# Performance work log

Measured on AMD Instinct MI355X. Metric: run time of the kernel, lower is better.

Reference implementation:

```python
import math
import jax, jax.numpy as jnp
import numpy as np

N = 50000      # nodes
E = 600000     # edges (before self-loops)
D_IN = 64
COND = 32
B = 50         # cond batch; N % B == 0
DT = 128       # dim_t
DH = 128       # dim_h
L = 3          # num GAT layers
FD = 16        # learned_sinusoidal_dim


def setup_inputs() -> dict:
    key = jax.random.key(0)
    ks = jax.random.split(key, 32)
    p = lambda k, shp: (jax.random.normal(k, shp, jnp.float32) * 0.05)
    return {
        "x": jax.random.normal(ks[0], (N, D_IN), jnp.float32),
        "adj": jax.random.randint(ks[1], (2, E), 0, N, dtype=jnp.int32),
        "ef": jax.random.normal(ks[2], (E, 8), jnp.float32),
        "timesteps": jax.random.uniform(ks[3], (N,), jnp.float32) * 1000.0,
        "cond": jax.random.normal(ks[4], (B, COND), jnp.float32),
        # random fourier weights (fixed, not trained in original since is_random=True)
        "fourier_w": jax.random.normal(ks[5], (FD // 2,), jnp.float32),
        # time MLP: Linear(FD+1, DT) -> SiLU -> Linear(DT, DT)
        "tW1": p(ks[6], (FD + 1, DT)), "tb1": p(ks[7], (DT,)),
        "tW2": p(ks[8], (DT, DT)),   "tb2": p(ks[9], (DT,)),
        # conditional projections
        "pxW": p(ks[10], (D_IN, DT)), "pxb": p(ks[11], (DT,)),
        "pcW": p(ks[12], (COND, DT)), "pcb": p(ks[13], (DT,)),
        # stacked GATConv params (all layers 128->128, heads=1)
        "linW": p(ks[14], (L, DT, DH)),   # lin, bias=False
        "attS": p(ks[15], (L, DH)),       # att_src
        "attD": p(ks[16], (L, DH)),       # att_dst
        "gbias": p(ks[17], (L, DH)),      # GATConv bias
        "resW": p(ks[18], (L, DT, DH)),   # residual Linear, bias=False
        # decode MLP
        "dW1": p(ks[19], (DH, DH)), "db1": p(ks[20], (DH,)),
        "dW2": p(ks[21], (DH, 2)),  "db2": p(ks[22], (2,)),
    }


def _gat_layer(h, src, dst, n, linW, attS, attD, gbias, resW):
    # PyG GATConv, heads=1, concat=True, residual=True, add_self_loops already in src/dst
    xl = h @ linW                          # [n, DH]
    a_src = xl @ attS                      # [n]
    a_dst = xl @ attD                      # [n]
    e = jax.nn.leaky_relu(a_src[src] + a_dst[dst], 0.2)   # [E2]
    m = jax.ops.segment_max(e, dst, num_segments=n)
    w = jnp.exp(e - m[dst])
    den = jax.ops.segment_sum(w, dst, num_segments=n)
    alpha = w / den[dst]                   # softmax per destination node
    out = jax.ops.segment_sum(alpha[:, None] * xl[src], dst, num_segments=n)
    return out + gbias + h @ resW


def reference(x, adj, ef, timesteps, cond, fourier_w, tW1, tb1, tW2, tb2,
              pxW, pxb, pcW, pcb, linW, attS, attD, gbias, resW,
              dW1, db1, dW2, db2):
    n = x.shape[0]
    # time embedding: random fourier features, dim = FD + 1
    t = timesteps[:, None]
    freqs = t * fourier_w[None, :] * (2.0 * math.pi)
    four = jnp.concatenate([t, jnp.sin(freqs), jnp.cos(freqs)], axis=-1)
    temb = jax.nn.silu(four @ tW1 + tb1) @ tW2 + tb2
    # conditional projection (cond repeated to match nodes)
    c = jnp.repeat(cond, n // cond.shape[0], axis=0)
    h = (x @ pxW + pxb) + (c @ pcW + pcb) + temb
    # add self-loops once (PyG GATConv default add_self_loops=True)
    loop = jnp.arange(n, dtype=adj.dtype)
    src = jnp.concatenate([adj[0], loop])
    dst = jnp.concatenate([adj[1], loop])
    for l in range(linW.shape[0]):
        h = _gat_layer(h, src, dst, n, linW[l], attS[l], attD[l], gbias[l], resW[l])
        h = jax.nn.gelu(h, approximate=False)
    # decode MLP
    h = jax.nn.gelu(h @ dW1 + db1, approximate=False)
    return h @ dW2 + db2
```

## Files before the change

### kernel.cpp

```cpp
#include <hip/hip_runtime.h>
#include <hip/hip_bf16.h>

#define N_NODES 50000
#define N_EDGES 600000
#define TOT_EDGES (N_EDGES + N_NODES)
#define NPB 1000
#define SCAN_BLK 49

#define PREP_T0 1563
#define PREP_T1 (PREP_T0 + 544)
#define PREP_T2 (PREP_T1 + 3125)
#define PREP_T3 (PREP_T2 + 25)
#define PREP_T4 (PREP_T3 + 3)

typedef __bf16 bf16x8 __attribute__((ext_vector_type(8)));
typedef float f32x4 __attribute__((ext_vector_type(4)));
typedef unsigned short u16x8 __attribute__((ext_vector_type(8)));

__device__ __forceinline__ float gelu_exact(float v){
  return 0.5f * v * (1.f + erff(v * 0.70710678118654752f));
}
__device__ __forceinline__ float silu(float v){
  return v / (1.f + expf(-v));
}
__device__ __forceinline__ unsigned short f2bf(float f){
  unsigned u = __builtin_bit_cast(unsigned, f);
  unsigned r = (u + 0x7FFFu + ((u >> 16) & 1u)) >> 16;
  return (unsigned short)r;
}
__device__ __forceinline__ float bf2f(unsigned short u){
  return __builtin_bit_cast(float, ((unsigned)u) << 16);
}

__global__ __launch_bounds__(256) void count_deg(const int* __restrict__ adj,
                                                 int* __restrict__ counts,
                                                 int* __restrict__ rank){
  int t = blockIdx.x*256 + threadIdx.x;
  if (t >= N_EDGES/4) return;
  int j4 = t*4;
  const int4 d4 = *(const int4*)&adj[N_EDGES + j4];
  int4 r4;
  r4.x = atomicAdd(&counts[d4.x], 1);
  r4.y = atomicAdd(&counts[d4.y], 1);
  r4.z = atomicAdd(&counts[d4.z], 1);
  r4.w = atomicAdd(&counts[d4.w], 1);
  *(int4*)&rank[j4] = r4;
}

__global__ __launch_bounds__(256) void scan_part(const int* __restrict__ counts, int* __restrict__ blksum){
  int tid = threadIdx.x;
  int base = blockIdx.x*1024 + tid*4;
  int s = 0;
  #pragma unroll
  for (int k = 0; k < 4; k++){ int idx = base+k; if (idx < N_NODES) s += counts[idx] + 1; }
  #pragma unroll
  for (int off = 1; off < 64; off <<= 1) s += __shfl_xor(s, off, 64);
  __shared__ int ws[4];
  int lane = tid & 63, wid = tid >> 6;
  if (lane == 0) ws[wid] = s;
  __syncthreads();
  if (tid == 0) blksum[blockIdx.x] = ws[0]+ws[1]+ws[2]+ws[3];
}

__global__ __launch_bounds__(256) void scan_final(const int* __restrict__ counts,
                                                  const int* __restrict__ blksum,
                                                  int* __restrict__ offsets,
                                                  int* __restrict__ srt_src){
  int tid = threadIdx.x; int lane = tid & 63, wid = tid >> 6;
  __shared__ int ws[4];
  __shared__ int sbase;
  int base = blockIdx.x*1024 + tid*4;
  int v[4]; int s = 0;
  #pragma unroll
  for (int k = 0; k < 4; k++){ int idx = base+k; v[k] = (idx < N_NODES) ? (counts[idx] + 1) : 0; s += v[k]; }
  int x = s;
  #pragma unroll
  for (int off = 1; off < 64; off <<= 1){
    int y = __shfl_up(x, off, 64);
    if (lane >= off) x += y;
  }
  if (lane == 63) ws[wid] = x;
  if (tid < 64){
    int bv = (tid < SCAN_BLK) ? blksum[tid] : 0;
    int bx = bv;
    #pragma unroll
    for (int off = 1; off < 64; off <<= 1){
      int y = __shfl_up(bx, off, 64);
      if (tid >= off) bx += y;
    }
    int basev = (blockIdx.x == 0) ? 0 : __shfl(bx, blockIdx.x - 1, 64);
    int total = __shfl(bx, SCAN_BLK - 1, 64);
    if (tid == 0){
      sbase = basev;
      if (blockIdx.x == SCAN_BLK-1) offsets[N_NODES] = total;
    }
  }
  __syncthreads();
  int run = sbase;
  for (int q = 0; q < wid; q++) run += ws[q];
  run += x - s;
  #pragma unroll
  for (int k = 0; k < 4; k++){
    int idx = base+k;
    if (idx < N_NODES){
      offsets[idx] = run;
      srt_src[run] = idx;
    }
    run += v[k];
  }
}

__global__ __launch_bounds__(256) void scatter_edges(const int* __restrict__ adj,
                                                     const int* __restrict__ rank,
                                                     const int* __restrict__ offsets,
                                                     int* __restrict__ srt_src){
  int t = blockIdx.x*256 + threadIdx.x;
  if (t >= N_EDGES/4) return;
  int j4 = t*4;
  const int4 s4 = *(const int4*)&adj[j4];
  const int4 d4 = *(const int4*)&adj[N_EDGES + j4];
  const int4 r4 = *(const int4*)&rank[j4];
  srt_src[offsets[d4.x] + 1 + r4.x] = s4.x;
  srt_src[offsets[d4.y] + 1 + r4.y] = s4.y;
  srt_src[offsets[d4.z] + 1 + r4.z] = s4.z;
  srt_src[offsets[d4.w] + 1 + r4.w] = s4.w;
}

__global__ __launch_bounds__(256) void prep_all(const float* __restrict__ timesteps,
                                                const float* __restrict__ fw,
                                                const float* __restrict__ tW1,
                                                const float* __restrict__ tb1,
                                                unsigned short* __restrict__ hid,
                                                const float* __restrict__ linW,
                                                const float* __restrict__ resW,
                                                const float* __restrict__ tW2,
                                                const float* __restrict__ pxW,
                                                const float* __restrict__ dW1,
                                                unsigned short* __restrict__ Bt2,
                                                unsigned short* __restrict__ Bt_init,
                                                unsigned short* __restrict__ Bt_d1,
                                                const float* __restrict__ x,
                                                unsigned short* __restrict__ xbf,
                                                const float* __restrict__ cond,
                                                const float* __restrict__ pcW,
                                                const float* __restrict__ pcb,
                                                float* __restrict__ cproj,
                                                const float* __restrict__ attS,
                                                const float* __restrict__ attD,
                                                float* __restrict__ uv){
  __shared__ float sfour[32][17];
  __shared__ float sW[17][128];
  const int bid = blockIdx.x, tid = threadIdx.x;

  if (bid < PREP_T0){
    int row0 = bid * 32;
    if (tid < 32){
      int gr = row0 + tid;
      float t = (gr < N_NODES) ? timesteps[gr] : 0.f;
      sfour[tid][0] = t;
      #pragma unroll
      for (int q = 0; q < 8; q++){
        float f = t * fw[q] * 6.2831853071795864769f;
        float sv, cv;
        sincosf(f, &sv, &cv);
        sfour[tid][1+q] = sv;
        sfour[tid][9+q] = cv;
      }
    }
    for (int i = tid; i < 17*128; i += 256) sW[i>>7][i&127] = tW1[i];
    __syncthreads();
    int j = tid & 127, rg = tid >> 7;
    float b = tb1[j];
    #pragma unroll
    for (int r = 0; r < 16; r++){
      int row = rg*16 + r;
      float acc = b;
      #pragma unroll
      for (int k = 0; k < 17; k++) acc += sfour[row][k]*sW[k][j];
      int gr = row0 + row;
      if (gr < N_NODES) hid[gr*128 + j] = f2bf(silu(acc));
    }
  } else if (bid < PREP_T1){
    int idx = (bid - PREP_T0)*256 + tid;
    if (idx < 98304){
      int j = idx >> 14, e = idx & 16383;
      int l = j >> 1, isres = j & 1;
      int k = e >> 7, c = e & 127;
      const float* src = (isres ? resW : linW) + l*16384;
      Bt2[(size_t)l*32768 + (size_t)(isres*128 + c)*128 + k] = f2bf(src[k*128 + c]);
    } else if (idx < 114688){
      int e = idx - 98304; int k = e >> 7, c = e & 127;
      Bt_init[c*192 + k] = f2bf(tW2[k*128 + c]);
    } else if (idx < 122880){
      int e = idx - 114688; int k = e >> 7, c = e & 127;
      Bt_init[c*192 + 128 + k] = f2bf(pxW[k*128 + c]);
    } else if (idx < 139264){
      int e = idx - 122880; int k = e >> 7, c = e & 127;
      Bt_d1[c*128 + k] = f2bf(dW1[k*128 + c]);
    }
  } else if (bid < PREP_T2){
    int i = (bid - PREP_T1)*256 + tid;
    float4 v = ((const float4*)x)[i];
    ushort4 o;
    o.x = f2bf(v.x); o.y = f2bf(v.y); o.z = f2bf(v.z); o.w = f2bf(v.w);
    *(ushort4*)&xbf[(size_t)i*4] = o;
  } else if (bid < PREP_T3){
    int g = (bid - PREP_T2)*256 + tid;
    int b = g >> 7, j = g & 127;
    float acc = pcb[j];
    for (int k = 0; k < 32; k++) acc += cond[b*32+k]*pcW[k*128+j];
    cproj[b*128+j] = acc;
  } else {
    int g = (bid - PREP_T3)*256 + tid;
    if (g < 768){
      int l = g >> 8, s = (g >> 7) & 1, k = g & 127;
      const float* att = s ? (attD + l*128) : (attS + l*128);
      const float* row = linW + (l*128 + k)*128;
      float acc = 0.f;
      for (int j = 0; j < 128; j++) acc += row[j]*att[j];
      uv[(l*2 + s)*128 + k] = acc;
    }
  }
}

template<int KD, int NC, int EPI, bool DOTS>
__global__ __launch_bounds__(256) void mfma_gemm(const unsigned short* __restrict__ A0,
                                                 const unsigned short* __restrict__ A1,
                                                 const unsigned short* __restrict__ Bt,
                                                 const float* __restrict__ bias0,
                                                 const float* __restrict__ bias1,
                                                 const float* __restrict__ cproj,
                                                 unsigned short* __restrict__ O0,
                                                 unsigned short* __restrict__ O1,
                                                 const float* __restrict__ uv_l,
                                                 float* __restrict__ a_srcO,
                                                 float* __restrict__ a_dstO){
  constexpr int CHR  = KD / 8;
  constexpr int ROWB = KD * 2;
  constexpr int KS   = KD / 32;
  constexpr int NT   = NC / 16;
  __shared__ alignas(16) char sA[64 * ROWB];
  __shared__ alignas(16) char sB[NC * ROWB];
  const int tid  = threadIdx.x;
  const int m0   = blockIdx.x * 64;
  const int lane = tid & 63, w = tid >> 6;
  const int lr   = lane & 15, lk = lane >> 4;

  for (int i = tid; i < 64*CHR; i += 256){
    int r = i / CHR, ch = i % CHR;
    int grow = m0 + r;
    u16x8 v;
    #pragma unroll
    for (int q = 0; q < 8; q++) v[q] = 0;
    if (grow < N_NODES){
      if constexpr (KD == 128){
        v = *(const u16x8*)&A0[(size_t)grow*128 + ch*8];
      } else {
        if (ch < 16) v = *(const u16x8*)&A0[(size_t)grow*128 + ch*8];
        else         v = *(const u16x8*)&A1[(size_t)grow*64 + (ch-16)*8];
      }
    }
    *(u16x8*)&sA[r*ROWB + ((ch*16) ^ ((r & 7) << 4))] = v;
  }
  for (int i = tid; i < NC*CHR; i += 256){
    int r = i / CHR, ch = i % CHR;
    u16x8 v = *(const u16x8*)&Bt[(size_t)r*KD + ch*8];
    *(u16x8*)&sB[r*ROWB + ((ch*16) ^ ((r & 7) << 4))] = v;
  }
  __syncthreads();

  bf16x8 afr[KS];
  const int arow = w*16 + lr;
  #pragma unroll
  for (int ks = 0; ks < KS; ks++)
    afr[ks] = *(const bf16x8*)&sA[arow*ROWB + ((ks*64 + lk*16) ^ ((arow & 7) << 4))];

  f32x4 acc[NT];
  #pragma unroll
  for (int nt = 0; nt < NT; nt++)
    #pragma unroll
    for (int q = 0; q < 4; q++) acc[nt][q] = 0.f;

  #pragma unroll
  for (int nt = 0; nt < NT; nt++){
    const int brow = nt*16 + lr;
    #pragma unroll
    for (int ks = 0; ks < KS; ks++){
      bf16x8 b = *(const bf16x8*)&sB[brow*ROWB + ((ks*64 + lk*16) ^ ((brow & 7) << 4))];
      acc[nt] = __builtin_amdgcn_mfma_f32_16x16x32_bf16(afr[ks], b, acc[nt], 0, 0, 0);
    }
  }

  if constexpr (DOTS){
    int r = tid >> 2;
    int row = m0 + r;
    if (row < N_NODES){
      float ps = 0.f, pd = 0.f;
      #pragma unroll
      for (int cc = 0; cc < 4; cc++){
        int ch = (tid & 3)*4 + cc;
        u16x8 av = *(const u16x8*)&sA[r*ROWB + ((ch*16) ^ ((r & 7) << 4))];
        int c0 = ch*8;
        const float4 u0 = *(const float4*)&uv_l[c0];
        const float4 u1 = *(const float4*)&uv_l[c0+4];
        const float4 v0 = *(const float4*)&uv_l[128+c0];
        const float4 v1 = *(const float4*)&uv_l[128+c0+4];
        const float uu[8] = {u0.x,u0.y,u0.z,u0.w,u1.x,u1.y,u1.z,u1.w};
        const float vv[8] = {v0.x,v0.y,v0.z,v0.w,v1.x,v1.y,v1.z,v1.w};
        #pragma unroll
        for (int q = 0; q < 8; q++){
          float hv = bf2f(av[q]);
          ps += hv*uu[q];
          pd += hv*vv[q];
        }
      }
      ps += __shfl_xor(ps, 1, 64); ps += __shfl_xor(ps, 2, 64);
      pd += __shfl_xor(pd, 1, 64); pd += __shfl_xor(pd, 2, 64);
      if ((tid & 3) == 0){ a_srcO[row] = ps; a_dstO[row] = pd; }
    }
  }

  const int rbase = m0 + w*16 + lk*4;
  #pragma unroll
  for (int nt = 0; nt < NT; nt++){
    int c = nt*16 + lr;
    #pragma unroll
    for (int rg = 0; rg < 4; rg++){
      int row = rbase + rg;
      if (row >= N_NODES) continue;
      float v = acc[nt][rg];
      if constexpr (EPI == 0){
        if (c < 128) O0[(size_t)row*128 + c]       = f2bf(v);
        else         O1[(size_t)row*128 + (c-128)] = f2bf(v);
      } else if constexpr (EPI == 1){
        v += bias0[c] + bias1[c] + cproj[(row/NPB)*128 + c];
        O0[(size_t)row*128 + c] = f2bf(v);
      } else {
        v = gelu_exact(v + bias0[c]);
        O0[(size_t)row*128 + c] = f2bf(v);
      }
    }
  }
}

template<bool FUSE>
__global__ __launch_bounds__(256) void aggregate(const unsigned short* __restrict__ xl,
                                                 const float* __restrict__ a_src,
                                                 const float* __restrict__ a_dst,
                                                 const unsigned short* __restrict__ hres,
                                                 const float* __restrict__ gbias_l,
                                                 const int* __restrict__ offsets,
                                                 const int* __restrict__ srt_src,
                                                 unsigned short* __restrict__ h_out,
                                                 const float* __restrict__ uv_next,
                                                 float* __restrict__ a_src_o,
                                                 float* __restrict__ a_dst_o){
  const int tid  = threadIdx.x;
  const int lane = tid & 63;
  const int l16  = lane & 15;
  const int i    = blockIdx.x*16 + (tid >> 4);
  const int beg  = offsets[i];
  const int deg  = offsets[i+1] - beg;
  const float adst = a_dst[i];

  int   s0  = 0;
  float ev0 = -INFINITY;
  if (l16 < deg){
    s0 = srt_src[beg + l16];
    float t = a_src[s0] + adst;
    ev0 = (t > 0.f) ? t : 0.2f*t;
  }
  float m = ev0;
  #pragma unroll
  for (int off = 1; off < 16; off <<= 1) m = fmaxf(m, __shfl_xor(m, off, 64));
  float den = (l16 < deg) ? __expf(ev0 - m) : 0.f;
  #pragma unroll
  for (int off = 1; off < 16; off <<= 1) den += __shfl_xor(den, off, 64);
  for (int c0 = 16; c0 < deg; c0 += 16){
    float ev = -INFINITY;
    if (c0 + l16 < deg){
      int s = srt_src[beg + c0 + l16];
      float t = a_src[s] + adst;
      ev = (t > 0.f) ? t : 0.2f*t;
    }
    float cm = ev;
    #pragma unroll
    for (int off = 1; off < 16; off <<= 1) cm = fmaxf(cm, __shfl_xor(cm, off, 64));
    if (cm > m){ den *= __expf(m - cm); m = cm; }
    float wv = (c0 + l16 < deg) ? __expf(ev - m) : 0.f;
    #pragma unroll
    for (int off = 1; off < 16; off <<= 1) wv += __shfl_xor(wv, off, 64);
    den += wv;
  }
  const float inv = 1.f / den;
  float w0 = (l16 < deg) ? __expf(ev0 - m) * inv : 0.f;

  float acc[8];
  #pragma unroll
  for (int k = 0; k < 8; k++) acc[k] = 0.f;
  const int gbb = (lane & 48) << 2;

  int lim0 = deg < 16 ? deg : 16;
  for (int q = 0; q < lim0; q++){
    int addr = gbb + q*4;
    int s    = __builtin_amdgcn_ds_bpermute(addr, s0);
    float wq = __builtin_bit_cast(float, __builtin_amdgcn_ds_bpermute(addr, __builtin_bit_cast(int, w0)));
    const int4 xv = *(const int4*)&xl[((size_t)s << 7) + (l16 << 3)];
    const int xd[4] = {xv.x, xv.y, xv.z, xv.w};
    #pragma unroll
    for (int k = 0; k < 4; k++){
      acc[2*k]   += wq * __builtin_bit_cast(float, xd[k] << 16);
      acc[2*k+1] += wq * __builtin_bit_cast(float, xd[k] & 0xffff0000);
    }
  }
  for (int c0 = 16; c0 < deg; c0 += 16){
    int s1 = 0; float w1 = 0.f;
    if (c0 + l16 < deg){
      s1 = srt_src[beg + c0 + l16];
      float t = a_src[s1] + adst;
      float ev = (t > 0.f) ? t : 0.2f*t;
      w1 = __expf(ev - m) * inv;
    }
    int lim = deg - c0; if (lim > 16) lim = 16;
    for (int q = 0; q < lim; q++){
      int addr = gbb + q*4;
      int s    = __builtin_amdgcn_ds_bpermute(addr, s1);
      float wq = __builtin_bit_cast(float, __builtin_amdgcn_ds_bpermute(addr, __builtin_bit_cast(int, w1)));
      const int4 xv = *(const int4*)&xl[((size_t)s << 7) + (l16 << 3)];
      const int xd[4] = {xv.x, xv.y, xv.z, xv.w};
      #pragma unroll
      for (int k = 0; k < 4; k++){
        acc[2*k]   += wq * __builtin_bit_cast(float, xd[k] << 16);
        acc[2*k+1] += wq * __builtin_bit_cast(float, xd[k] & 0xffff0000);
      }
    }
  }

  const int4 hr = *(const int4*)&hres[((size_t)i << 7) + (l16 << 3)];
  const int hd[4] = {hr.x, hr.y, hr.z, hr.w};
  const float4 gb0 = *(const float4*)&gbias_l[l16*8];
  const float4 gb1 = *(const float4*)&gbias_l[l16*8 + 4];
  const float gbv[8] = {gb0.x, gb0.y, gb0.z, gb0.w, gb1.x, gb1.y, gb1.z, gb1.w};
  float uu[8], vv[8];
  if constexpr (FUSE){
    const float4 a0 = *(const float4*)&uv_next[l16*8];
    const float4 a1 = *(const float4*)&uv_next[l16*8 + 4];
    const float4 b0 = *(const float4*)&uv_next[128 + l16*8];
    const float4 b1 = *(const float4*)&uv_next[128 + l16*8 + 4];
    uu[0]=a0.x; uu[1]=a0.y; uu[2]=a0.z; uu[3]=a0.w; uu[4]=a1.x; uu[5]=a1.y; uu[6]=a1.z; uu[7]=a1.w;
    vv[0]=b0.x; vv[1]=b0.y; vv[2]=b0.z; vv[3]=b0.w; vv[4]=b1.x; vv[5]=b1.y; vv[6]=b1.z; vv[7]=b1.w;
  }
  float ps = 0.f, pd = 0.f;
  int od[4];
  #pragma unroll
  for (int k = 0; k < 4; k++){
    float r0 = acc[2*k]   + gbv[2*k]   + __builtin_bit_cast(float, hd[k] << 16);
    float r1 = acc[2*k+1] + gbv[2*k+1] + __builtin_bit_cast(float, hd[k] & 0xffff0000);
    float g0 = gelu_exact(r0);
    float g1 = gelu_exact(r1);
    if constexpr (FUSE){
      ps += g0*uu[2*k] + g1*uu[2*k+1];
      pd += g0*vv[2*k] + g1*vv[2*k+1];
    }
    unsigned lo = f2bf(g0);
    unsigned hi = f2bf(g1);
    od[k] = (int)(lo | (hi << 16));
  }
  *(int4*)&h_out[((size_t)i << 7) + (l16 << 3)] = make_int4(od[0], od[1], od[2], od[3]);
  if constexpr (FUSE){
    #pragma unroll
    for (int off = 1; off < 16; off <<= 1){
      ps += __shfl_xor(ps, off, 64);
      pd += __shfl_xor(pd, off, 64);
    }
    if (l16 == 0){ a_src_o[i] = ps; a_dst_o[i] = pd; }
  }
}

__global__ __launch_bounds__(256) void head2(const unsigned short* __restrict__ g,
                                             const float* __restrict__ dW2,
                                             const float* __restrict__ db2,
                                             float* __restrict__ out){
  const int tid = threadIdx.x;
  const int l16 = tid & 15;
  const int i   = blockIdx.x*16 + (tid >> 4);
  const int4 gv = *(const int4*)&g[((size_t)i << 7) + (l16 << 3)];
  const int gd[4] = {gv.x, gv.y, gv.z, gv.w};
  float wk[16];
  #pragma unroll
  for (int q = 0; q < 4; q++){
    const float4 wq = *(const float4*)&dW2[l16*16 + q*4];
    wk[q*4+0]=wq.x; wk[q*4+1]=wq.y; wk[q*4+2]=wq.z; wk[q*4+3]=wq.w;
  }
  float p0 = 0.f, p1 = 0.f;
  #pragma unroll
  for (int k = 0; k < 4; k++){
    float lo = __builtin_bit_cast(float, gd[k] << 16);
    float hi = __builtin_bit_cast(float, gd[k] & 0xffff0000);
    p0 += lo*wk[4*k+0] + hi*wk[4*k+2];
    p1 += lo*wk[4*k+1] + hi*wk[4*k+3];
  }
  #pragma unroll
  for (int off = 1; off < 16; off <<= 1){
    p0 += __shfl_xor(p0, off, 64);
    p1 += __shfl_xor(p1, off, 64);
  }
  if (l16 == 0){
    float2 o; o.x = p0 + db2[0]; o.y = p1 + db2[1];
    *(float2*)&out[i*2] = o;
  }
}

extern "C" void kernel_launch(void* const* d_in, const int* in_sizes, int n_in,
                              void* d_out, int out_size, void* d_ws, size_t ws_size,
                              hipStream_t stream) {
  const float* x   = (const float*)d_in[0];
  const int*   adj = (const int*)  d_in[1];
  const float* timesteps = (const float*)d_in[3];
  const float* cond = (const float*)d_in[4];
  const float* fw   = (const float*)d_in[5];
  const float* tW1  = (const float*)d_in[6];
  const float* tb1  = (const float*)d_in[7];
  const float* tW2  = (const float*)d_in[8];
  const float* tb2  = (const float*)d_in[9];
  const float* pxW  = (const float*)d_in[10];
  const float* pxb  = (const float*)d_in[11];
  const float* pcW  = (const float*)d_in[12];
  const float* pcb  = (const float*)d_in[13];
  const float* linW = (const float*)d_in[14];
  const float* attS = (const float*)d_in[15];
  const float* attD = (const float*)d_in[16];
  const float* gbias= (const float*)d_in[17];
  const float* resW = (const float*)d_in[18];
  const float* dW1  = (const float*)d_in[19];
  const float* db1  = (const float*)d_in[20];
  const float* dW2  = (const float*)d_in[21];
  const float* db2  = (const float*)d_in[22];
  float* out = (float*)d_out;

  char* w = (char*)d_ws;
  size_t off = 0;
  auto carve = [&](size_t bytes) -> void* {
    void* p = w + off;
    off = (off + bytes + 255) & ~(size_t)255;
    return p;
  };
  unsigned short* h_bf    = (unsigned short*)carve((size_t)N_NODES*128*2);
  unsigned short* xl_bf   = (unsigned short*)carve((size_t)N_NODES*128*2);
  unsigned short* hres_bf = (unsigned short*)carve((size_t)N_NODES*128*2);
  unsigned short* x_bf    = (unsigned short*)carve((size_t)N_NODES*64*2);
  float* a_src0 = (float*)carve((size_t)N_NODES*4);
  float* a_dst0 = (float*)carve((size_t)N_NODES*4);
  float* a_src1 = (float*)carve((size_t)N_NODES*4);
  float* a_dst1 = (float*)carve((size_t)N_NODES*4);
  float* cproj = (float*)carve(50*128*4);
  float* uv    = (float*)carve(6*128*4);
  int* counts  = (int*)carve((size_t)N_NODES*4);
  int* rank    = (int*)carve((size_t)N_EDGES*4);
  int* offsets = (int*)carve((size_t)(N_NODES+1)*4);
  int* srt_src = (int*)carve((size_t)TOT_EDGES*4);
  int* blksum  = (int*)carve(SCAN_BLK*4);
  unsigned short* Bt2     = (unsigned short*)carve((size_t)3*256*128*2);
  unsigned short* Bt_init = (unsigned short*)carve((size_t)128*192*2);
  unsigned short* Bt_d1   = (unsigned short*)carve((size_t)128*128*2);
  (void)ws_size; (void)in_sizes; (void)n_in; (void)out_size;

  const int edge4_blocks = (N_EDGES/4 + 255)/256;
  const int gemm_gx      = (N_NODES + 63)/64;
  const int grp_blocks   = N_NODES/16;

  hipMemsetAsync(counts, 0, (size_t)N_NODES*4, stream);
  count_deg<<<edge4_blocks, 256, 0, stream>>>(adj, counts, rank);
  scan_part<<<SCAN_BLK, 256, 0, stream>>>(counts, blksum);
  scan_final<<<SCAN_BLK, 256, 0, stream>>>(counts, blksum, offsets, srt_src);
  scatter_edges<<<edge4_blocks, 256, 0, stream>>>(adj, rank, offsets, srt_src);

  prep_all<<<PREP_T4, 256, 0, stream>>>(timesteps, fw, tW1, tb1, xl_bf ,
                                        linW, resW, tW2, pxW, dW1, Bt2, Bt_init, Bt_d1,
                                        x, x_bf, cond, pcW, pcb, cproj, attS, attD, uv);

  mfma_gemm<192,128,1,false><<<gemm_gx, 256, 0, stream>>>(xl_bf , x_bf, Bt_init, tb2, pxb, cproj, h_bf, nullptr, nullptr, nullptr, nullptr);

  float* asrc_in = a_src0; float* adst_in = a_dst0;
  float* asrc_out = a_src1; float* adst_out = a_dst1;
  for (int l = 0; l < 3; l++){
    if (l == 0){
      mfma_gemm<128,256,0,true><<<gemm_gx, 256, 0, stream>>>(h_bf, nullptr, Bt2, nullptr, nullptr, nullptr, xl_bf, hres_bf, uv, asrc_in, adst_in);
    } else {
      mfma_gemm<128,256,0,false><<<gemm_gx, 256, 0, stream>>>(h_bf, nullptr, Bt2 + (size_t)l*32768, nullptr, nullptr, nullptr, xl_bf, hres_bf, nullptr, nullptr, nullptr);
    }
    if (l < 2){
      aggregate<true><<<grp_blocks, 256, 0, stream>>>(xl_bf, asrc_in, adst_in, hres_bf, gbias + l*128,
                                                      offsets, srt_src, h_bf, uv + (l+1)*256, asrc_out, adst_out);
      float* t0 = asrc_in; asrc_in = asrc_out; asrc_out = t0;
      float* t1 = adst_in; adst_in = adst_out; adst_out = t1;
    } else {
      aggregate<false><<<grp_blocks, 256, 0, stream>>>(xl_bf, asrc_in, adst_in, hres_bf, gbias + l*128,
                                                       offsets, srt_src, h_bf, nullptr, nullptr, nullptr);
    }
  }

  mfma_gemm<128,128,2,false><<<gemm_gx, 256, 0, stream>>>(h_bf, nullptr, Bt_d1, db1, nullptr, nullptr, xl_bf , nullptr, nullptr, nullptr, nullptr);
  head2<<<grp_blocks, 256, 0, stream>>>(xl_bf , dW2, db2, out);
}
```

Measured before the change: 409.7 us.

## Merge edge counting into prep, scatter into init GEMM, head into decode GEMM

Degree counting now runs as extra blocks of the prep kernel, and the edge scatter runs as extra blocks of the initial projection GEMM launch. The final decode GEMM gains an epilogue that applies GELU and the 128->2 projection in registers, which removes the separate head kernel and the bf16 round-trip of the decoded hidden state. The aim is fewer launches and less global traffic. The cost is more heterogeneous blocks per launch and larger kernel parameter lists.

```diff
diff --git a/kernel.cpp b/kernel.cpp
--- a/kernel.cpp
+++ b/kernel.cpp
@@ -6,12 +6,14 @@
 #define TOT_EDGES (N_EDGES + N_NODES)
 #define NPB 1000
 #define SCAN_BLK 49
-
-#define PREP_T0 1563
-#define PREP_T1 (PREP_T0 + 544)
-#define PREP_T2 (PREP_T1 + 3125)
-#define PREP_T3 (PREP_T2 + 25)
-#define PREP_T4 (PREP_T3 + 3)
+#define GEMM_GX 782
+#define CD_BLKS 586
+
+#define PC_T0 (CD_BLKS + 1563)
+#define PC_T1 (PC_T0 + 544)
+#define PC_T2 (PC_T1 + 3125)
+#define PC_T3 (PC_T2 + 25)
+#define PC_T4 (PC_T3 + 3)
 
 typedef __bf16 bf16x8 __attribute__((ext_vector_type(8)));
 typedef float f32x4 __attribute__((ext_vector_type(4)));
@@ -32,128 +34,49 @@
   return __builtin_bit_cast(float, ((unsigned)u) << 16);
 }
 
-__global__ __launch_bounds__(256) void count_deg(const int* __restrict__ adj,
-                                                 int* __restrict__ counts,
-                                                 int* __restrict__ rank){
-  int t = blockIdx.x*256 + threadIdx.x;
-  if (t >= N_EDGES/4) return;
-  int j4 = t*4;
-  const int4 d4 = *(const int4*)&adj[N_EDGES + j4];
-  int4 r4;
-  r4.x = atomicAdd(&counts[d4.x], 1);
-  r4.y = atomicAdd(&counts[d4.y], 1);
-  r4.z = atomicAdd(&counts[d4.z], 1);
-  r4.w = atomicAdd(&counts[d4.w], 1);
-  *(int4*)&rank[j4] = r4;
-}
-
-__global__ __launch_bounds__(256) void scan_part(const int* __restrict__ counts, int* __restrict__ blksum){
-  int tid = threadIdx.x;
-  int base = blockIdx.x*1024 + tid*4;
-  int s = 0;
-  #pragma unroll
-  for (int k = 0; k < 4; k++){ int idx = base+k; if (idx < N_NODES) s += counts[idx] + 1; }
-  #pragma unroll
-  for (int off = 1; off < 64; off <<= 1) s += __shfl_xor(s, off, 64);
-  __shared__ int ws[4];
-  int lane = tid & 63, wid = tid >> 6;
-  if (lane == 0) ws[wid] = s;
-  __syncthreads();
-  if (tid == 0) blksum[blockIdx.x] = ws[0]+ws[1]+ws[2]+ws[3];
-}
-
-__global__ __launch_bounds__(256) void scan_final(const int* __restrict__ counts,
-                                                  const int* __restrict__ blksum,
-                                                  int* __restrict__ offsets,
-                                                  int* __restrict__ srt_src){
-  int tid = threadIdx.x; int lane = tid & 63, wid = tid >> 6;
-  __shared__ int ws[4];
-  __shared__ int sbase;
-  int base = blockIdx.x*1024 + tid*4;
-  int v[4]; int s = 0;
-  #pragma unroll
-  for (int k = 0; k < 4; k++){ int idx = base+k; v[k] = (idx < N_NODES) ? (counts[idx] + 1) : 0; s += v[k]; }
-  int x = s;
-  #pragma unroll
-  for (int off = 1; off < 64; off <<= 1){
-    int y = __shfl_up(x, off, 64);
-    if (lane >= off) x += y;
-  }
-  if (lane == 63) ws[wid] = x;
-  if (tid < 64){
-    int bv = (tid < SCAN_BLK) ? blksum[tid] : 0;
-    int bx = bv;
-    #pragma unroll
-    for (int off = 1; off < 64; off <<= 1){
-      int y = __shfl_up(bx, off, 64);
-      if (tid >= off) bx += y;
-    }
-    int basev = (blockIdx.x == 0) ? 0 : __shfl(bx, blockIdx.x - 1, 64);
-    int total = __shfl(bx, SCAN_BLK - 1, 64);
-    if (tid == 0){
-      sbase = basev;
-      if (blockIdx.x == SCAN_BLK-1) offsets[N_NODES] = total;
-    }
-  }
-  __syncthreads();
-  int run = sbase;
-  for (int q = 0; q < wid; q++) run += ws[q];
-  run += x - s;
-  #pragma unroll
-  for (int k = 0; k < 4; k++){
-    int idx = base+k;
-    if (idx < N_NODES){
-      offsets[idx] = run;
-      srt_src[run] = idx;
-    }
-    run += v[k];
-  }
-}
-
-__global__ __launch_bounds__(256) void scatter_edges(const int* __restrict__ adj,
-                                                     const int* __restrict__ rank,
-                                                     const int* __restrict__ offsets,
-                                                     int* __restrict__ srt_src){
-  int t = blockIdx.x*256 + threadIdx.x;
-  if (t >= N_EDGES/4) return;
-  int j4 = t*4;
-  const int4 s4 = *(const int4*)&adj[j4];
-  const int4 d4 = *(const int4*)&adj[N_EDGES + j4];
-  const int4 r4 = *(const int4*)&rank[j4];
-  srt_src[offsets[d4.x] + 1 + r4.x] = s4.x;
-  srt_src[offsets[d4.y] + 1 + r4.y] = s4.y;
-  srt_src[offsets[d4.z] + 1 + r4.z] = s4.z;
-  srt_src[offsets[d4.w] + 1 + r4.w] = s4.w;
-}
-
-__global__ __launch_bounds__(256) void prep_all(const float* __restrict__ timesteps,
-                                                const float* __restrict__ fw,
-                                                const float* __restrict__ tW1,
-                                                const float* __restrict__ tb1,
-                                                unsigned short* __restrict__ hid,
-                                                const float* __restrict__ linW,
-                                                const float* __restrict__ resW,
-                                                const float* __restrict__ tW2,
-                                                const float* __restrict__ pxW,
-                                                const float* __restrict__ dW1,
-                                                unsigned short* __restrict__ Bt2,
-                                                unsigned short* __restrict__ Bt_init,
-                                                unsigned short* __restrict__ Bt_d1,
-                                                const float* __restrict__ x,
-                                                unsigned short* __restrict__ xbf,
-                                                const float* __restrict__ cond,
-                                                const float* __restrict__ pcW,
-                                                const float* __restrict__ pcb,
-                                                float* __restrict__ cproj,
-                                                const float* __restrict__ attS,
-                                                const float* __restrict__ attD,
-                                                float* __restrict__ uv){
+__global__ __launch_bounds__(256) void prep_count(const int* __restrict__ adj,
+                                                  int* __restrict__ counts,
+                                                  int* __restrict__ rank,
+                                                  const float* __restrict__ timesteps,
+                                                  const float* __restrict__ fw,
+                                                  const float* __restrict__ tW1,
+                                                  const float* __restrict__ tb1,
+                                                  unsigned short* __restrict__ hid,
+                                                  const float* __restrict__ linW,
+                                                  const float* __restrict__ resW,
+                                                  const float* __restrict__ tW2,
+                                                  const float* __restrict__ pxW,
+                                                  const float* __restrict__ dW1,
+                                                  unsigned short* __restrict__ Bt2,
+                                                  unsigned short* __restrict__ Bt_init,
+                                                  unsigned short* __restrict__ Bt_d1,
+                                                  const float* __restrict__ x,
+                                                  unsigned short* __restrict__ xbf,
+                                                  const float* __restrict__ cond,
+                                                  const float* __restrict__ pcW,
+                                                  const float* __restrict__ pcb,
+                                                  float* __restrict__ cproj,
+                                                  const float* __restrict__ attS,
+                                                  const float* __restrict__ attD,
+                                                  float* __restrict__ uv){
   __shared__ float sfour[32][17];
   __shared__ float sW[17][128];
   const int bid = blockIdx.x, tid = threadIdx.x;
 
-  if (bid < PREP_T0){
-    int row0 = bid * 32;
+  if (bid < CD_BLKS){
+    int t = bid*256 + tid;
+    if (t < N_EDGES/4){
+      int j4 = t*4;
+      const int4 d4 = *(const int4*)&adj[N_EDGES + j4];
+      int4 r4;
+      r4.x = atomicAdd(&counts[d4.x], 1);
+      r4.y = atomicAdd(&counts[d4.y], 1);
+      r4.z = atomicAdd(&counts[d4.z], 1);
+      r4.w = atomicAdd(&counts[d4.w], 1);
+      *(int4*)&rank[j4] = r4;
+    }
+  } else if (bid < PC_T0){
+    int row0 = (bid - CD_BLKS) * 32;
     if (tid < 32){
       int gr = row0 + tid;
       float t = (gr < N_NODES) ? timesteps[gr] : 0.f;
@@ -180,8 +103,8 @@
       int gr = row0 + row;
       if (gr < N_NODES) hid[gr*128 + j] = f2bf(silu(acc));
     }
-  } else if (bid < PREP_T1){
-    int idx = (bid - PREP_T0)*256 + tid;
+  } else if (bid < PC_T1){
+    int idx = (bid - PC_T0)*256 + tid;
     if (idx < 98304){
       int j = idx >> 14, e = idx & 16383;
       int l = j >> 1, isres = j & 1;
@@ -198,20 +121,20 @@
       int e = idx - 122880; int k = e >> 7, c = e & 127;
       Bt_d1[c*128 + k] = f2bf(dW1[k*128 + c]);
     }
-  } else if (bid < PREP_T2){
-    int i = (bid - PREP_T1)*256 + tid;
+  } else if (bid < PC_T2){
+    int i = (bid - PC_T1)*256 + tid;
     float4 v = ((const float4*)x)[i];
     ushort4 o;
     o.x = f2bf(v.x); o.y = f2bf(v.y); o.z = f2bf(v.z); o.w = f2bf(v.w);
     *(ushort4*)&xbf[(size_t)i*4] = o;
-  } else if (bid < PREP_T3){
-    int g = (bid - PREP_T2)*256 + tid;
+  } else if (bid < PC_T3){
+    int g = (bid - PC_T2)*256 + tid;
     int b = g >> 7, j = g & 127;
     float acc = pcb[j];
     for (int k = 0; k < 32; k++) acc += cond[b*32+k]*pcW[k*128+j];
     cproj[b*128+j] = acc;
   } else {
-    int g = (bid - PREP_T3)*256 + tid;
+    int g = (bid - PC_T3)*256 + tid;
     if (g < 768){
       int l = g >> 8, s = (g >> 7) & 1, k = g & 127;
       const float* att = s ? (attD + l*128) : (attS + l*128);
@@ -223,7 +146,70 @@
   }
 }
 
-template<int KD, int NC, int EPI, bool DOTS>
+__global__ __launch_bounds__(256) void scan_part(const int* __restrict__ counts, int* __restrict__ blksum){
+  int tid = threadIdx.x;
+  int base = blockIdx.x*1024 + tid*4;
+  int s = 0;
+  #pragma unroll
+  for (int k = 0; k < 4; k++){ int idx = base+k; if (idx < N_NODES) s += counts[idx] + 1; }
+  #pragma unroll
+  for (int off = 1; off < 64; off <<= 1) s += __shfl_xor(s, off, 64);
+  __shared__ int ws[4];
+  int lane = tid & 63, wid = tid >> 6;
+  if (lane == 0) ws[wid] = s;
+  __syncthreads();
+  if (tid == 0) blksum[blockIdx.x] = ws[0]+ws[1]+ws[2]+ws[3];
+}
+
+__global__ __launch_bounds__(256) void scan_final(const int* __restrict__ counts,
+                                                  const int* __restrict__ blksum,
+                                                  int* __restrict__ offsets,
+                                                  int* __restrict__ srt_src){
+  int tid = threadIdx.x; int lane = tid & 63, wid = tid >> 6;
+  __shared__ int ws[4];
+  __shared__ int sbase;
+  int base = blockIdx.x*1024 + tid*4;
+  int v[4]; int s = 0;
+  #pragma unroll
+  for (int k = 0; k < 4; k++){ int idx = base+k; v[k] = (idx < N_NODES) ? (counts[idx] + 1) : 0; s += v[k]; }
+  int x = s;
+  #pragma unroll
+  for (int off = 1; off < 64; off <<= 1){
+    int y = __shfl_up(x, off, 64);
+    if (lane >= off) x += y;
+  }
+  if (lane == 63) ws[wid] = x;
+  if (tid < 64){
+    int bv = (tid < SCAN_BLK) ? blksum[tid] : 0;
+    int bx = bv;
+    #pragma unroll
+    for (int off = 1; off < 64; off <<= 1){
+      int y = __shfl_up(bx, off, 64);
+      if (tid >= off) bx += y;
+    }
+    int basev = (blockIdx.x == 0) ? 0 : __shfl(bx, blockIdx.x - 1, 64);
+    int total = __shfl(bx, SCAN_BLK - 1, 64);
+    if (tid == 0){
+      sbase = basev;
+      if (blockIdx.x == SCAN_BLK-1) offsets[N_NODES] = total;
+    }
+  }
+  __syncthreads();
+  int run = sbase;
+  for (int q = 0; q < wid; q++) run += ws[q];
+  run += x - s;
+  #pragma unroll
+  for (int k = 0; k < 4; k++){
+    int idx = base+k;
+    if (idx < N_NODES){
+      offsets[idx] = run;
+      srt_src[run] = idx;
+    }
+    run += v[k];
+  }
+}
+
+template<int KD, int NC, int EPI, bool DOTS, bool SCAT>
 __global__ __launch_bounds__(256) void mfma_gemm(const unsigned short* __restrict__ A0,
                                                  const unsigned short* __restrict__ A1,
                                                  const unsigned short* __restrict__ Bt,
@@ -234,7 +220,12 @@
                                                  unsigned short* __restrict__ O1,
                                                  const float* __restrict__ uv_l,
                                                  float* __restrict__ a_srcO,
-                                                 float* __restrict__ a_dstO){
+                                                 float* __restrict__ a_dstO,
+                                                 float* __restrict__ fout,
+                                                 const int* __restrict__ adj,
+                                                 const int* __restrict__ rank,
+                                                 const int* __restrict__ offsets,
+                                                 int* __restrict__ srt_src){
   constexpr int CHR  = KD / 8;
   constexpr int ROWB = KD * 2;
   constexpr int KS   = KD / 32;
@@ -242,6 +233,24 @@
   __shared__ alignas(16) char sA[64 * ROWB];
   __shared__ alignas(16) char sB[NC * ROWB];
   const int tid  = threadIdx.x;
+
+  if constexpr (SCAT){
+    if (blockIdx.x >= GEMM_GX){
+      int t = (blockIdx.x - GEMM_GX)*256 + tid;
+      if (t < N_EDGES/4){
+        int j4 = t*4;
+        const int4 s4 = *(const int4*)&adj[j4];
+        const int4 d4 = *(const int4*)&adj[N_EDGES + j4];
+        const int4 r4 = *(const int4*)&rank[j4];
+        srt_src[offsets[d4.x] + 1 + r4.x] = s4.x;
+        srt_src[offsets[d4.y] + 1 + r4.y] = s4.y;
+        srt_src[offsets[d4.z] + 1 + r4.z] = s4.z;
+        srt_src[offsets[d4.w] + 1 + r4.w] = s4.w;
+      }
+      return;
+    }
+  }
+
   const int m0   = blockIdx.x * 64;
   const int lane = tid & 63, w = tid >> 6;
   const int lr   = lane & 15, lk = lane >> 4;
@@ -321,23 +330,57 @@
   }
 
   const int rbase = m0 + w*16 + lk*4;
-  #pragma unroll
-  for (int nt = 0; nt < NT; nt++){
-    int c = nt*16 + lr;
-    #pragma unroll
-    for (int rg = 0; rg < 4; rg++){
-      int row = rbase + rg;
-      if (row >= N_NODES) continue;
-      float v = acc[nt][rg];
-      if constexpr (EPI == 0){
-        if (c < 128) O0[(size_t)row*128 + c]       = f2bf(v);
-        else         O1[(size_t)row*128 + (c-128)] = f2bf(v);
-      } else if constexpr (EPI == 1){
-        v += bias0[c] + bias1[c] + cproj[(row/NPB)*128 + c];
-        O0[(size_t)row*128 + c] = f2bf(v);
-      } else {
-        v = gelu_exact(v + bias0[c]);
-        O0[(size_t)row*128 + c] = f2bf(v);
+  if constexpr (EPI < 3){
+    #pragma unroll
+    for (int nt = 0; nt < NT; nt++){
+      int c = nt*16 + lr;
+      #pragma unroll
+      for (int rg = 0; rg < 4; rg++){
+        int row = rbase + rg;
+        if (row >= N_NODES) continue;
+        float v = acc[nt][rg];
+        if constexpr (EPI == 0){
+          if (c < 128) O0[(size_t)row*128 + c]       = f2bf(v);
+          else         O1[(size_t)row*128 + (c-128)] = f2bf(v);
+        } else if constexpr (EPI == 1){
+          v += bias0[c] + bias1[c] + cproj[(row/NPB)*128 + c];
+          O0[(size_t)row*128 + c] = f2bf(v);
+        } else {
+          v = gelu_exact(v + bias0[c]);
+          O0[(size_t)row*128 + c] = f2bf(v);
+        }
+      }
+    }
+  } else {
+    float p0[4] = {0.f,0.f,0.f,0.f}, p1[4] = {0.f,0.f,0.f,0.f};
+    #pragma unroll
+    for (int nt = 0; nt < NT; nt++){
+      int c = nt*16 + lr;
+      const float2 wv = *(const float2*)&cproj[c*2];
+      #pragma unroll
+      for (int rg = 0; rg < 4; rg++){
+        float g = gelu_exact(acc[nt][rg] + bias0[c]);
+        p0[rg] += g * wv.x;
+        p1[rg] += g * wv.y;
+      }
+    }
+    #pragma unroll
+    for (int off = 1; off < 16; off <<= 1){
+      #pragma unroll
+      for (int rg = 0; rg < 4; rg++){
+        p0[rg] += __shfl_xor(p0[rg], off, 64);
+        p1[rg] += __shfl_xor(p1[rg], off, 64);
+      }
+    }
+    if (lr == 0){
+      float b0 = bias1[0], b1 = bias1[1];
+      #pragma unroll
+      for (int rg = 0; rg < 4; rg++){
+        int row = rbase + rg;
+        if (row < N_NODES){
+          float2 o; o.x = p0[rg] + b0; o.y = p1[rg] + b1;
+          *(float2*)&fout[row*2] = o;
+        }
       }
     }
   }
@@ -474,40 +517,6 @@
       pd += __shfl_xor(pd, off, 64);
     }
     if (l16 == 0){ a_src_o[i] = ps; a_dst_o[i] = pd; }
-  }
-}
-
-__global__ __launch_bounds__(256) void head2(const unsigned short* __restrict__ g,
-                                             const float* __restrict__ dW2,
-                                             const float* __restrict__ db2,
-                                             float* __restrict__ out){
-  const int tid = threadIdx.x;
-  const int l16 = tid & 15;
-  const int i   = blockIdx.x*16 + (tid >> 4);
-  const int4 gv = *(const int4*)&g[((size_t)i << 7) + (l16 << 3)];
-  const int gd[4] = {gv.x, gv.y, gv.z, gv.w};
-  float wk[16];
-  #pragma unroll
-  for (int q = 0; q < 4; q++){
-    const float4 wq = *(const float4*)&dW2[l16*16 + q*4];
-    wk[q*4+0]=wq.x; wk[q*4+1]=wq.y; wk[q*4+2]=wq.z; wk[q*4+3]=wq.w;
-  }
-  float p0 = 0.f, p1 = 0.f;
-  #pragma unroll
-  for (int k = 0; k < 4; k++){
-    float lo = __builtin_bit_cast(float, gd[k] << 16);
-    float hi = __builtin_bit_cast(float, gd[k] & 0xffff0000);
-    p0 += lo*wk[4*k+0] + hi*wk[4*k+2];
-    p1 += lo*wk[4*k+1] + hi*wk[4*k+3];
-  }
-  #pragma unroll
-  for (int off = 1; off < 16; off <<= 1){
-    p0 += __shfl_xor(p0, off, 64);
-    p1 += __shfl_xor(p1, off, 64);
-  }
-  if (l16 == 0){
-    float2 o; o.x = p0 + db2[0]; o.y = p1 + db2[1];
-    *(float2*)&out[i*2] = o;
   }
 }
 
@@ -565,29 +574,33 @@
   unsigned short* Bt_d1   = (unsigned short*)carve((size_t)128*128*2);
   (void)ws_size; (void)in_sizes; (void)n_in; (void)out_size;
 
-  const int edge4_blocks = (N_EDGES/4 + 255)/256;
-  const int gemm_gx      = (N_NODES + 63)/64;
-  const int grp_blocks   = N_NODES/16;
+  const int grp_blocks = N_NODES/16;
 
   hipMemsetAsync(counts, 0, (size_t)N_NODES*4, stream);
-  count_deg<<<edge4_blocks, 256, 0, stream>>>(adj, counts, rank);
+
+  prep_count<<<PC_T4, 256, 0, stream>>>(adj, counts, rank,
+                                        timesteps, fw, tW1, tb1, xl_bf ,
+                                        linW, resW, tW2, pxW, dW1, Bt2, Bt_init, Bt_d1,
+                                        x, x_bf, cond, pcW, pcb, cproj, attS, attD, uv);
+
   scan_part<<<SCAN_BLK, 256, 0, stream>>>(counts, blksum);
   scan_final<<<SCAN_BLK, 256, 0, stream>>>(counts, blksum, offsets, srt_src);
-  scatter_edges<<<edge4_blocks, 256, 0, stream>>>(adj, rank, offsets, srt_src);
-
-  prep_all<<<PREP_T4, 256, 0, stream>>>(timesteps, fw, tW1, tb1, xl_bf ,
-                                        linW, resW, tW2, pxW, dW1, Bt2, Bt_init, Bt_d1,
-                                        x, x_bf, cond, pcW, pcb, cproj, attS, attD, uv);
-
-  mfma_gemm<192,128,1,false><<<gemm_gx, 256, 0, stream>>>(xl_bf , x_bf, Bt_init, tb2, pxb, cproj, h_bf, nullptr, nullptr, nullptr, nullptr);
+
+  mfma_gemm<192,128,1,false,true><<<GEMM_GX + CD_BLKS, 256, 0, stream>>>(
+      xl_bf , x_bf, Bt_init, tb2, pxb, cproj, h_bf, nullptr,
+      nullptr, nullptr, nullptr, nullptr, adj, rank, offsets, srt_src);
 
   float* asrc_in = a_src0; float* adst_in = a_dst0;
   float* asrc_out = a_src1; float* adst_out = a_dst1;
   for (int l = 0; l < 3; l++){
     if (l == 0){
-      mfma_gemm<128,256,0,true><<<gemm_gx, 256, 0, stream>>>(h_bf, nullptr, Bt2, nullptr, nullptr, nullptr, xl_bf, hres_bf, uv, asrc_in, adst_in);
+      mfma_gemm<128,256,0,true,false><<<GEMM_GX, 256, 0, stream>>>(
+          h_bf, nullptr, Bt2, nullptr, nullptr, nullptr, xl_bf, hres_bf,
+          uv, asrc_in, adst_in, nullptr, nullptr, nullptr, nullptr, nullptr);
     } else {
-      mfma_gemm<128,256,0,false><<<gemm_gx, 256, 0, stream>>>(h_bf, nullptr, Bt2 + (size_t)l*32768, nullptr, nullptr, nullptr, xl_bf, hres_bf, nullptr, nullptr, nullptr);
+      mfma_gemm<128,256,0,false,false><<<GEMM_GX, 256, 0, stream>>>(
+          h_bf, nullptr, Bt2 + (size_t)l*32768, nullptr, nullptr, nullptr, xl_bf, hres_bf,
+          nullptr, nullptr, nullptr, nullptr, nullptr, nullptr, nullptr, nullptr);
     }
     if (l < 2){
       aggregate<true><<<grp_blocks, 256, 0, stream>>>(xl_bf, asrc_in, adst_in, hres_bf, gbias + l*128,
@@ -600,6 +613,7 @@
     }
   }
 
-  mfma_gemm<128,128,2,false><<<gemm_gx, 256, 0, stream>>>(h_bf, nullptr, Bt_d1, db1, nullptr, nullptr, xl_bf , nullptr, nullptr, nullptr, nullptr);
-  head2<<<grp_blocks, 256, 0, stream>>>(xl_bf , dW2, db2, out);
-}
+  mfma_gemm<128,128,3,false,false><<<GEMM_GX, 256, 0, stream>>>(
+      h_bf, nullptr, Bt_d1, db1, db2, dW2, nullptr, nullptr,
+      nullptr, nullptr, nullptr, out, nullptr, nullptr, nullptr, nullptr);
+}
```

New measurement: 387.6 us. -5.4%, faster.
